# Kernel optimization log

Measured on AMD Instinct MI355X. Metric: run time of the kernel, lower is better.

## Reference

```python
import jax, jax.numpy as jnp
import numpy as np

N_NODES = 1024
N_FEAT = 12        # must equal LOOKBACK (U1 @ B @ U2.T constraint in original code)
LOOKBACK = 12
N_DATA = 8
KSIZE = 2
DILATIONS = [1, 3, 3, 3]
DELTA_MIN = 0.05
TIME_FEATS = 36    # 15 + 5 + 4 + 12


def setup_inputs() -> dict:
    key = jax.random.key(0)
    ks = jax.random.split(key, 21)
    f32 = jnp.float32

    def rn(k, shape, fan_in):
        return jax.random.normal(k, shape, dtype=f32) / np.sqrt(fan_in)

    return {
        'observation': jax.random.normal(ks[0], (N_NODES, N_DATA, LOOKBACK), dtype=f32),
        'time_features': jax.random.normal(ks[1], (TIME_FEATS,), dtype=f32),
        # main FC stack: (n_nodes*n_data) -> fc1 -> fc2 -> n_nodes*n_feat
        'fc_w1': rn(ks[2], (N_NODES * N_DATA, 2048), N_NODES * N_DATA),
        'fc_b1': jnp.zeros((2048,), f32),
        'fc_w2': rn(ks[3], (2048, 2048), 2048),
        'fc_b2': jnp.zeros((2048,), f32),
        'fc_w3': rn(ks[4], (2048, N_NODES * N_FEAT), 2048),
        'fc_b3': jnp.zeros((N_NODES * N_FEAT,), f32),
        # graph conv weights
        'W_forward': rn(ks[5], (KSIZE, N_FEAT, N_FEAT), N_FEAT),
        'W_backward': rn(ks[6], (KSIZE, N_FEAT, N_FEAT), N_FEAT),
        'b': jnp.zeros((N_FEAT,), f32),
        # GraphConstructor params (one fixed set, reused for every adjacency)
        'layer_initial': rn(ks[7], (LOOKBACK, N_NODES), N_NODES),
        'gs_w1': rn(ks[8], (N_NODES, 256), N_NODES),
        'gs_b1': jnp.zeros((256,), f32),
        'gs_w2': rn(ks[9], (256, N_NODES * N_FEAT), 256),
        'gs_b2': jnp.zeros((N_NODES * N_FEAT,), f32),
        'gt_w1': rn(ks[10], (TIME_FEATS, 256), TIME_FEATS),
        'gt_b1': jnp.zeros((256,), f32),
        'gt_w2': rn(ks[11], (256, N_NODES * N_FEAT), 256),
        'gt_b2': jnp.zeros((N_NODES * N_FEAT,), f32),
        'B': jax.random.normal(ks[12], (N_FEAT, N_FEAT), dtype=f32) / N_FEAT,
    }


def _forward(observation, time_features, fc_w1, fc_b1, fc_w2, fc_b2, fc_w3, fc_b3,
             W_forward, W_backward, b, layer_initial,
             gs_w1, gs_b1, gs_w2, gs_b2, gt_w1, gt_b1, gt_w2, gt_b2, B):
    relu = jax.nn.relu

    # fully_connected: observation (N, D, L) -> X (N, F, L)
    obs = jnp.transpose(observation, (2, 0, 1)).reshape(LOOKBACK, -1)  # (L, N*D)
    h = relu(obs @ fc_w1 + fc_b1)
    h = relu(h @ fc_w2 + fc_b2)
    h = relu(h @ fc_w3 + fc_b3)                                        # (L, N*F)
    X0 = jnp.transpose(h.reshape(LOOKBACK, N_NODES, N_FEAT), (1, 2, 0))  # (N, F, L)

    # node embedding U (N, L, F), computed once (graph params fixed)
    sp = relu(relu(layer_initial @ gs_w1 + gs_b1) @ gs_w2 + gs_b2)     # (L, N*F)
    tp = relu(relu(time_features @ gt_w1 + gt_b1) @ gt_w2 + gt_b2)     # (N*F,)
    U = jnp.transpose((sp + tp).reshape(LOOKBACK, N_NODES, N_FEAT), (1, 0, 2))

    adj_cache = {}

    def norm_adj(a, c):
        # normalized adjacency between feature-slices a and c (static ints)
        if (a, c) in adj_cache:
            return adj_cache[(a, c)]
        U1 = U[:, :, a]                      # (N, L)
        U2 = U[:, :, c]                      # (N, L)
        x = U1 @ B @ U2.T                    # (N, N); valid since L == F
        x = jnp.where(x >= DELTA_MIN, x, 0.0)
        A = jax.nn.softmax(x, axis=1)        # torch F.softmax default dim=1 for 2D
        # degree = diag(rowsum); inv(sqrtm(diag)) = diag(1/sqrt(rowsum))
        d = 1.0 / jnp.sqrt(A.sum(-1))
        out = A * d[:, None] * d[None, :]
        adj_cache[(a, c)] = out
        return out

    def conv(X, t):
        Z = jnp.zeros((N_NODES, N_FEAT), jnp.float32)
        for k in range(KSIZE):
            X_t = X[:, :, t - k]             # (N, F)
            L1 = norm_adj(t - k, t)
            L2 = norm_adj(t + k, t)
            x = L1 @ X_t @ W_forward[k] + L2 @ X_t @ W_backward[k] + b
            Z = Z + jax.nn.relu(x)
        return Z

    def conv_layer(X, d):
        cols = []
        for t in range(1, LOOKBACK - 1):
            if t % d == 0:
                cols.append(conv(X, t))
            else:
                cols.append(jnp.zeros((N_NODES, N_FEAT), jnp.float32))
        return jnp.stack(cols, axis=-1)      # (N, F, L-2)

    Z0 = conv_layer(X0, DILATIONS[0])
    Z1 = conv_layer(Z0, DILATIONS[1])
    Z2 = conv_layer(Z1, DILATIONS[2])
    Z3 = conv_layer(Z2, DILATIONS[3])
    return (Z0[:, :, -1], Z1[:, :, -1], Z2[:, :, -1], Z3[:, :, -1])


def reference(observation, time_features, fc_w1, fc_b1, fc_w2, fc_b2, fc_w3, fc_b3,
              W_forward, W_backward, b, layer_initial,
              gs_w1, gs_b1, gs_w2, gs_b2, gt_w1, gt_b1, gt_w2, gt_b2, B):
    return _forward(observation, time_features, fc_w1, fc_b1, fc_w2, fc_b2, fc_w3, fc_b3,
                    W_forward, W_backward, b, layer_initial,
                    gs_w1, gs_b1, gs_w2, gs_b2, gt_w1, gt_b1, gt_w2, gt_b2, B)
```

## Files before the change

kernel.cpp:

```cpp
#include <hip/hip_runtime.h>


#define OFF_SPP   0
#define OFF_TPH   49152
#define OFF_P1    65536
#define OFF_P2    196608
#define OFF_P3    262144
#define OFF_UP    393216
#define OFF_TPP   1572864
#define OFF_U     1703936
#define OFF_Y     1740800

template<int KS, int PIN, int P, int GATHER>
__device__ __forceinline__ void gemm_body(
    const float* __restrict__ xin, const float* __restrict__ bias_in,
    const float* __restrict__ W, float* __restrict__ part,
    int N, int K, int bx, int by, float* lx, float* red)
{
  int tid = threadIdx.x;
  int k0 = by * KS;
  for (int i = tid; i < 2*KS; i += 256) {
    int t = i / KS, kk = i - t*KS;
    float v;
    if (GATHER) {
      int k = k0 + kk;
      v = xin[(k >> 3)*96 + (k & 7)*12 + 9 + t];
    } else if (PIN == 0) {
      v = xin[t*K + k0 + kk];
    } else {
      v = 0.f;
      const float* p0 = xin + (size_t)(t*K + k0 + kk)*PIN;
      #pragma unroll
      for (int p = 0; p < PIN; ++p) v += p0[p];
    }
    if (bias_in) { v += bias_in[k0 + kk]; v = v > 0.f ? v : 0.f; }
    lx[i] = v;
  }
  __syncthreads();
  int kg = tid >> 5, cg = tid & 31;
  int colbase = bx*128 + cg*4;
  float a0=0,a1=0,a2=0,a3=0,c0=0,c1=0,c2=0,c3=0;
  const int ksub = KS/8;
  for (int kk = kg*ksub; kk < kg*ksub + ksub; ++kk) {
    float4 w = *(const float4*)(W + (size_t)(k0+kk)*N + colbase);
    float x0 = lx[kk], x1 = lx[KS + kk];
    a0=fmaf(x0,w.x,a0); a1=fmaf(x0,w.y,a1); a2=fmaf(x0,w.z,a2); a3=fmaf(x0,w.w,a3);
    c0=fmaf(x1,w.x,c0); c1=fmaf(x1,w.y,c1); c2=fmaf(x1,w.z,c2); c3=fmaf(x1,w.w,c3);
  }
  float* rp = red + (kg*32 + cg)*8;
  rp[0]=a0; rp[1]=a1; rp[2]=a2; rp[3]=a3; rp[4]=c0; rp[5]=c1; rp[6]=c2; rp[7]=c3;
  __syncthreads();
  int cg2 = tid & 31, q = tid >> 5;
  float s = 0.f;
  #pragma unroll
  for (int g = 0; g < 8; ++g) s += red[(g*32 + cg2)*8 + q];
  int t = q >> 2, c = q & 3;
  part[(size_t)(t*N + bx*128 + cg2*4 + c)*P + by] = s;
}

template<int KS, int PIN, int P>
__global__ void __launch_bounds__(256) k_gemm(
    const float* __restrict__ xin, const float* __restrict__ bias_in,
    const float* __restrict__ W, float* __restrict__ part, int N, int K)
{
  __shared__ float lx[2*KS];
  __shared__ float red[2048];
  gemm_body<KS, PIN, P, 0>(xin, bias_in, W, part, N, K,
                           blockIdx.x, blockIdx.y, lx, red);
}

__global__ void __launch_bounds__(256) k_front(
    const float* __restrict__ obs, const float* __restrict__ fc_w1,
    float* __restrict__ part1,
    const float* __restrict__ li, const float* __restrict__ gs_w1,
    const float* __restrict__ tf, const float* __restrict__ gt_w1,
    const float* __restrict__ gt_b1,
    float* __restrict__ sp_part, float* __restrict__ tp_h)
{
  __shared__ float smem[2560];
  int b = blockIdx.x, tid = threadIdx.x;
  if (b < 512) {
    gemm_body<256, 0, 32, 1>(obs, (const float*)nullptr, fc_w1, part1,
                             2048, 8192, b & 15, b >> 4, smem, smem + 512);
  } else if (b < 528) {
    float (*lil)[128] = (float(*)[128])smem;
    int sb = b - 512;
    int cb = sb & 1, kc = sb >> 1;
    for (int i = tid; i < 1536; i += 256) {
      int bb = i >> 7, kk = i & 127;
      lil[bb][kk] = li[bb*1024 + kc*128 + kk];
    }
    __syncthreads();
    int col = cb*128 + (tid & 127);
    int kh = tid >> 7;
    float acc[12];
    #pragma unroll
    for (int t=0;t<12;++t) acc[t]=0.f;
    for (int kk = kh*64; kk < kh*64 + 64; ++kk) {
      float w = gs_w1[(size_t)(kc*128 + kk)*256 + col];
      #pragma unroll
      for (int t=0;t<12;++t) acc[t] = fmaf(lil[t][kk], w, acc[t]);
    }
    int c = kc*2 + kh;
    #pragma unroll
    for (int t=0;t<12;++t) sp_part[(c*12 + t)*256 + col] = acc[t];
  } else {
    float acc = 0.f;
    for (int k = 0; k < 36; ++k)
      acc = fmaf(tf[k], gt_w1[k*256 + tid], acc);
    float v = acc + gt_b1[tid];
    tp_h[tid] = v > 0.f ? v : 0.f;
  }
}

__global__ void __launch_bounds__(256) k_big(
    const float* __restrict__ part2, const float* __restrict__ fc_b2,
    const float* __restrict__ fc_w3, float* __restrict__ part3,
    const float* __restrict__ sp_part, const float* __restrict__ gs_b1,
    const float* __restrict__ tp_h,
    const float* __restrict__ gs_w2, const float* __restrict__ gt_w2,
    float* __restrict__ U_part, float* __restrict__ tp_part)
{
  __shared__ float smem[3072];
  int g = blockIdx.x, tid = threadIdx.x;
  if (g < 384) {
    gemm_body<512, 16, 4, 0>(part2, fc_b2, fc_w3, part3, 12288, 2048,
                             g >> 2, g & 3, smem, smem + 1024);
  } else {
    float* spl = smem;
    float* tpl = smem + 96;
    int ug = g - 384;
    int n  = (ug & 3)*256 + tid;
    int uy = ug >> 2;
    int k0 = uy*8;
    if (tid < 96) {
      int kk = tid / 12, t = tid % 12;
      float v = gs_b1[k0 + kk];
      #pragma unroll
      for (int c = 0; c < 16; ++c) v += sp_part[(c*12 + t)*256 + k0 + kk];
      spl[kk*12 + t] = v > 0.f ? v : 0.f;
    }
    if (tid < 8) tpl[tid] = tp_h[k0 + tid];
    __syncthreads();
    float sA[3][12];
    float tA[3] = {0.f, 0.f, 0.f};
    #pragma unroll
    for (int ap=0;ap<3;++ap)
      #pragma unroll
      for (int t=0;t<12;++t) sA[ap][t]=0.f;
    #pragma unroll
    for (int kk = 0; kk < 8; ++kk) {
      float4 ws4 = *(const float4*)(gs_w2 + (size_t)(k0+kk)*12288 + 12*n + 8);
      float4 wt4 = *(const float4*)(gt_w2 + (size_t)(k0+kk)*12288 + 12*n + 8);
      float w0 = ws4.y, w1 = ws4.z, w2 = ws4.w;
      #pragma unroll
      for (int t=0;t<12;++t) {
        float s = spl[kk*12 + t];
        sA[0][t] = fmaf(s, w0, sA[0][t]);
        sA[1][t] = fmaf(s, w1, sA[1][t]);
        sA[2][t] = fmaf(s, w2, sA[2][t]);
      }
      float tv = tpl[kk];
      tA[0] = fmaf(tv, wt4.y, tA[0]);
      tA[1] = fmaf(tv, wt4.z, tA[1]);
      tA[2] = fmaf(tv, wt4.w, tA[2]);
    }
    #pragma unroll
    for (int ap=0;ap<3;++ap) {
      #pragma unroll
      for (int t=0;t<12;++t)
        U_part[(size_t)uy*36864 + ap*12288 + n*12 + t] = sA[ap][t];
      tp_part[uy*3072 + n*3 + ap] = tA[ap];
    }
  }
}

__global__ void __launch_bounds__(256) k_mid(
    const float* __restrict__ U_part, const float* __restrict__ tp_part,
    const float* __restrict__ gs_b2, const float* __restrict__ gt_b2,
    float* __restrict__ U,
    const float* __restrict__ part3, const float* __restrict__ fc_b3,
    const float* __restrict__ Wf, const float* __restrict__ Wb,
    float* __restrict__ Y, float* __restrict__ out_tail)
{
  int b = blockIdx.x, tid = threadIdx.x;
  if (b < 144) {
    int i = b*256 + tid;
    float us = 0.f;
    for (int y = 0; y < 32; ++y) us += U_part[(size_t)y*36864 + i];
    int ap = i / 12288, rem = i - ap*12288, n = rem / 12;
    float ts = 0.f;
    for (int y = 0; y < 32; ++y) ts += tp_part[y*3072 + n*3 + ap];
    int c = n*12 + 9 + ap;
    float sv = us + gs_b2[c]; sv = sv > 0.f ? sv : 0.f;
    float tv = ts + gt_b2[c]; tv = tv > 0.f ? tv : 0.f;
    U[i] = sv + tv;
  } else if (b < 148) {
    __shared__ float Ws0[144], Ws1[144], Ws2[144];
    if (tid < 144) {
      Ws0[tid] = Wf[144 + tid];
      Ws1[tid] = Wf[tid] + Wb[tid];
      Ws2[tid] = Wb[144 + tid];
    }
    __syncthreads();
    int n = (b - 144)*256 + tid;
    float X9[12], X10[12];
    #pragma unroll
    for (int f=0; f<12; ++f) {
      float bb = fc_b3[n*12 + f];
      const float* p9  = part3 + (size_t)(n*12 + f)*4;
      const float* p10 = part3 + (size_t)(12288 + n*12 + f)*4;
      float v9 = bb, v10 = bb;
      #pragma unroll
      for (int p = 0; p < 4; ++p) { v9 += p9[p]; v10 += p10[p]; }
      X9[f]  = v9  > 0.f ? v9  : 0.f;
      X10[f] = v10 > 0.f ? v10 : 0.f;
    }
    #pragma unroll
    for (int g2=0; g2<12; ++g2) {
      float y0=0.f, y1=0.f, y2=0.f;
      #pragma unroll
      for (int f=0; f<12; ++f) {
        y0 = fmaf(X9[f],  Ws0[f*12+g2], y0);
        y1 = fmaf(X10[f], Ws1[f*12+g2], y1);
        y2 = fmaf(X9[f],  Ws2[f*12+g2], y2);
      }
      Y[n*12 + g2]         = y0;
      Y[12288 + n*12 + g2] = y1;
      Y[24576 + n*12 + g2] = y2;
    }
  } else {
    int i = (b - 148)*256 + tid;
    out_tail[i] = 0.f;
  }
}

#define SS 1032
__global__ void __launch_bounds__(256) k_final(
    const float* __restrict__ U, const float* __restrict__ Y,
    const float* __restrict__ Bm, const float* __restrict__ bvec,
    float* __restrict__ out)
{
  __shared__ float sc[6*SS];
  __shared__ float P[2][3][12];
  __shared__ float invS[6];
  __shared__ float Bl[144];
  __shared__ float bl[12];
  int tid = threadIdx.x;
  int i0 = blockIdx.x*2;
  if (tid < 144) Bl[tid] = Bm[tid];
  if (tid < 12)  bl[tid] = bvec[tid];
  __syncthreads();
  if (tid < 72) {
    int r = tid / 36, ap = (tid / 12) % 3, j = tid % 12;
    float s = 0.f;
    #pragma unroll
    for (int t=0;t<12;++t)
      s = fmaf(U[ap*12288 + (i0+r)*12 + t], Bl[t*12 + j], s);
    P[r][ap][j] = s;
  }
  __syncthreads();
  const float* U10 = U + 12288;
  for (int jj = 0; jj < 4; ++jj) {
    int j = tid + jj*256;
    const float4* ur = (const float4*)(U10 + j*12);
    float4 u0 = ur[0], u1 = ur[1], u2 = ur[2];
    float u[12] = {u0.x,u0.y,u0.z,u0.w,u1.x,u1.y,u1.z,u1.w,u2.x,u2.y,u2.z,u2.w};
    #pragma unroll
    for (int r=0;r<2;++r)
      #pragma unroll
      for (int ap=0;ap<3;++ap) {
        float s = 0.f;
        #pragma unroll
        for (int t=0;t<12;++t) s = fmaf(P[r][ap][t], u[t], s);
        sc[(r*3+ap)*SS + j] = (s >= 0.05f) ? s : 0.f;
      }
  }
  __syncthreads();
  int wv = tid >> 6, ln = tid & 63;
  for (int p = wv; p < 6; p += 4) {
    float m = -1e30f;
    for (int q = 0; q < 16; ++q) m = fmaxf(m, sc[p*SS + ln + q*64]);
    #pragma unroll
    for (int o = 32; o > 0; o >>= 1) m = fmaxf(m, __shfl_xor(m, o));
    float sum = 0.f;
    for (int q = 0; q < 16; ++q) {
      int j = ln + q*64;
      float e = __expf(sc[p*SS + j] - m);
      sc[p*SS + j] = e;
      sum += e;
    }
    #pragma unroll
    for (int o = 32; o > 0; o >>= 1) sum += __shfl_xor(sum, o);
    if (ln == 0) invS[p] = 1.f / sum;
  }
  __syncthreads();
  float acc[2][12];
  for (int r = 0; r < 2; ++r)
    for (int f = 0; f < 12; ++f)
      acc[r][f] = 0.f;
  int q3 = tid >> 6, jg = tid & 63;
  if (tid < 192) {
    for (int q = 0; q < 16; ++q) {
      int j = jg + q*64;
      const float4* yr = (const float4*)(Y + q3*12288 + j*12);
      float4 y0 = yr[0], y1 = yr[1], y2 = yr[2];
      float yv[12] = {y0.x,y0.y,y0.z,y0.w,y1.x,y1.y,y1.z,y1.w,y2.x,y2.y,y2.z,y2.w};
      float e0 = sc[(0*3+q3)*SS + j];
      float e1 = sc[(1*3+q3)*SS + j];
      #pragma unroll
      for (int f=0;f<12;++f) {
        acc[0][f] = fmaf(e0, yv[f], acc[0][f]);
        acc[1][f] = fmaf(e1, yv[f], acc[1][f]);
      }
    }
  }
  __syncthreads();
  float* red = sc;
  if (tid < 192) {
    #pragma unroll
    for (int r=0;r<2;++r)
      #pragma unroll
      for (int f=0;f<12;++f)
        red[((q3*2 + r)*12 + f)*64 + jg] = acc[r][f];
  }
  __syncthreads();
  if (tid < 24) {
    int r = tid / 12, f = tid % 12;
    float s0=0.f, s1=0.f, s2=0.f;
    for (int g = 0; g < 64; ++g) {
      s0 += red[((0*2+r)*12+f)*64 + g];
      s1 += red[((1*2+r)*12+f)*64 + g];
      s2 += red[((2*2+r)*12+f)*64 + g];
    }
    float a1v = invS[r*3+1]*s1;
    float a2v = invS[r*3+0]*s0 + invS[r*3+2]*s2;
    float v1 = a1v + bl[f]; v1 = v1>0.f ? v1 : 0.f;
    float v2 = a2v + bl[f]; v2 = v2>0.f ? v2 : 0.f;
    out[(i0+r)*12 + f] = v1 + v2;
  }
}

extern "C" void kernel_launch(void* const* d_in, const int* in_sizes, int n_in,
                              void* d_out, int out_size, void* d_ws, size_t ws_size,
                              hipStream_t stream)
{
  const float* obs   = (const float*)d_in[0];
  const float* tf    = (const float*)d_in[1];
  const float* fc_w1 = (const float*)d_in[2];
  const float* fc_b1 = (const float*)d_in[3];
  const float* fc_w2 = (const float*)d_in[4];
  const float* fc_b2 = (const float*)d_in[5];
  const float* fc_w3 = (const float*)d_in[6];
  const float* fc_b3 = (const float*)d_in[7];
  const float* Wf    = (const float*)d_in[8];
  const float* Wb    = (const float*)d_in[9];
  const float* bvec  = (const float*)d_in[10];
  const float* li    = (const float*)d_in[11];
  const float* gs_w1 = (const float*)d_in[12];
  const float* gs_b1 = (const float*)d_in[13];
  const float* gs_w2 = (const float*)d_in[14];
  const float* gs_b2 = (const float*)d_in[15];
  const float* gt_w1 = (const float*)d_in[16];
  const float* gt_b1 = (const float*)d_in[17];
  const float* gt_w2 = (const float*)d_in[18];
  const float* gt_b2 = (const float*)d_in[19];
  const float* Bm    = (const float*)d_in[20];
  float* out = (float*)d_out;
  float* ws  = (float*)d_ws;

  float* sp_part = ws + OFF_SPP;
  float* tp_h    = ws + OFF_TPH;
  float* part1   = ws + OFF_P1;
  float* part2   = ws + OFF_P2;
  float* part3   = ws + OFF_P3;
  float* U_part  = ws + OFF_UP;
  float* tp_part = ws + OFF_TPP;
  float* U       = ws + OFF_U;
  float* Y       = ws + OFF_Y;

  k_front<<<dim3(529), dim3(256), 0, stream>>>(obs, fc_w1, part1,
                                               li, gs_w1, tf, gt_w1, gt_b1,
                                               sp_part, tp_h);
  k_gemm<128, 32, 16><<<dim3(16,16), dim3(256), 0, stream>>>(
      part1, fc_b1, fc_w2, part2, 2048, 2048);
  k_big<<<dim3(512), dim3(256), 0, stream>>>(part2, fc_b2, fc_w3, part3,
                                             sp_part, gs_b1, tp_h,
                                             gs_w2, gt_w2, U_part, tp_part);
  k_mid<<<dim3(292), dim3(256), 0, stream>>>(U_part, tp_part, gs_b2, gt_b2, U,
                                             part3, fc_b3, Wf, Wb, Y,
                                             out + 12288);
  k_final<<<dim3(512), dim3(256), 0, stream>>>(U, Y, Bm, bvec, out);
}
```

Measured before the change: 294.7 us.

## Restructure pipeline into four kernels, fusing U computation and softmax with GEMMs

```diff
diff --git a/kernel.cpp b/kernel.cpp
--- a/kernel.cpp
+++ b/kernel.cpp
@@ -1,15 +1,13 @@
 #include <hip/hip_runtime.h>
-
 
 #define OFF_SPP   0
 #define OFF_TPH   49152
 #define OFF_P1    65536
 #define OFF_P2    196608
 #define OFF_P3    262144
-#define OFF_UP    393216
-#define OFF_TPP   1572864
 #define OFF_U     1703936
-#define OFF_Y     1740800
+#define OFF_E     1777664
+#define OFF_IS    4923392
 
 template<int KS, int PIN, int P, int GATHER>
 __device__ __forceinline__ void gemm_body(
@@ -31,14 +29,14 @@
       v = 0.f;
       const float* p0 = xin + (size_t)(t*K + k0 + kk)*PIN;
       #pragma unroll
-      for (int p = 0; p < PIN; ++p) v += p0[p];
+      for (int pp = 0; pp < PIN; ++pp) v += p0[pp];
     }
     if (bias_in) { v += bias_in[k0 + kk]; v = v > 0.f ? v : 0.f; }
     lx[i] = v;
   }
   __syncthreads();
-  int kg = tid >> 5, cg = tid & 31;
-  int colbase = bx*128 + cg*4;
+  int kg = tid >> 5, cg2 = tid & 31;
+  int colbase = bx*128 + cg2*4;
   float a0=0,a1=0,a2=0,a3=0,c0=0,c1=0,c2=0,c3=0;
   const int ksub = KS/8;
   for (int kk = kg*ksub; kk < kg*ksub + ksub; ++kk) {
@@ -47,26 +45,15 @@
     a0=fmaf(x0,w.x,a0); a1=fmaf(x0,w.y,a1); a2=fmaf(x0,w.z,a2); a3=fmaf(x0,w.w,a3);
     c0=fmaf(x1,w.x,c0); c1=fmaf(x1,w.y,c1); c2=fmaf(x1,w.z,c2); c3=fmaf(x1,w.w,c3);
   }
-  float* rp = red + (kg*32 + cg)*8;
+  float* rp = red + (kg*32 + cg2)*8;
   rp[0]=a0; rp[1]=a1; rp[2]=a2; rp[3]=a3; rp[4]=c0; rp[5]=c1; rp[6]=c2; rp[7]=c3;
   __syncthreads();
-  int cg2 = tid & 31, q = tid >> 5;
+  int cg3 = tid & 31, q = tid >> 5;
   float s = 0.f;
   #pragma unroll
-  for (int g = 0; g < 8; ++g) s += red[(g*32 + cg2)*8 + q];
+  for (int g = 0; g < 8; ++g) s += red[(g*32 + cg3)*8 + q];
   int t = q >> 2, c = q & 3;
-  part[(size_t)(t*N + bx*128 + cg2*4 + c)*P + by] = s;
-}
-
-template<int KS, int PIN, int P>
-__global__ void __launch_bounds__(256) k_gemm(
-    const float* __restrict__ xin, const float* __restrict__ bias_in,
-    const float* __restrict__ W, float* __restrict__ part, int N, int K)
-{
-  __shared__ float lx[2*KS];
-  __shared__ float red[2048];
-  gemm_body<KS, PIN, P, 0>(xin, bias_in, W, part, N, K,
-                           blockIdx.x, blockIdx.y, lx, red);
+  part[(size_t)(t*N + bx*128 + cg3*4 + c)*P + by] = s;
 }
 
 __global__ void __launch_bounds__(256) k_front(
@@ -75,7 +62,8 @@
     const float* __restrict__ li, const float* __restrict__ gs_w1,
     const float* __restrict__ tf, const float* __restrict__ gt_w1,
     const float* __restrict__ gt_b1,
-    float* __restrict__ sp_part, float* __restrict__ tp_h)
+    float* __restrict__ sp_part, float* __restrict__ tp_h,
+    float* __restrict__ out_tail)
 {
   __shared__ float smem[2560];
   int b = blockIdx.x, tid = threadIdx.x;
@@ -87,8 +75,8 @@
     int sb = b - 512;
     int cb = sb & 1, kc = sb >> 1;
     for (int i = tid; i < 1536; i += 256) {
-      int bb = i >> 7, kk = i & 127;
-      lil[bb][kk] = li[bb*1024 + kc*128 + kk];
+      int r = i >> 7, kk = i & 127;
+      lil[r][kk] = li[r*1024 + kc*128 + kk];
     }
     __syncthreads();
     int col = cb*128 + (tid & 127);
@@ -104,6 +92,7 @@
     int c = kc*2 + kh;
     #pragma unroll
     for (int t=0;t<12;++t) sp_part[(c*12 + t)*256 + col] = acc[t];
+    for (int i = tid; i < 2304; i += 256) out_tail[sb*2304 + i] = 0.f;
   } else {
     float acc = 0.f;
     for (int k = 0; k < 36; ++k)
@@ -113,210 +102,182 @@
   }
 }
 
-__global__ void __launch_bounds__(256) k_big(
-    const float* __restrict__ part2, const float* __restrict__ fc_b2,
-    const float* __restrict__ fc_w3, float* __restrict__ part3,
+__global__ void __launch_bounds__(256) k_umid(
+    const float* __restrict__ part1, const float* __restrict__ fc_b1,
+    const float* __restrict__ fc_w2, float* __restrict__ part2,
     const float* __restrict__ sp_part, const float* __restrict__ gs_b1,
     const float* __restrict__ tp_h,
     const float* __restrict__ gs_w2, const float* __restrict__ gt_w2,
-    float* __restrict__ U_part, float* __restrict__ tp_part)
-{
-  __shared__ float smem[3072];
-  int g = blockIdx.x, tid = threadIdx.x;
-  if (g < 384) {
+    const float* __restrict__ gs_b2, const float* __restrict__ gt_b2,
+    float* __restrict__ U)
+{
+  __shared__ float smem[3328];
+  int b = blockIdx.x, tid = threadIdx.x;
+  if (b < 256) {
+    gemm_body<128, 32, 16, 0>(part1, fc_b1, fc_w2, part2, 2048, 2048,
+                              b & 15, b >> 4, smem, smem + 256);
+    return;
+  }
+  float* spl = smem;
+  float* tpl = smem + 3072;
+  for (int i = tid; i < 3072; i += 256) {
+    int k = i / 12, t = i - k*12;
+    float v = gs_b1[k];
+    #pragma unroll
+    for (int c = 0; c < 16; ++c) v += sp_part[(c*12 + t)*256 + k];
+    spl[i] = v > 0.f ? v : 0.f;
+  }
+  tpl[tid] = tp_h[tid];
+  __syncthreads();
+  int grp = tid >> 5, l = tid & 31;
+  int n = (b - 256)*8 + grp;
+  int ap1 = l / 12, t1 = l - ap1*12;
+  bool has2 = (l < 7), sp2 = (l < 4);
+  int t2 = 8 + l;
+  const float* g1 = gs_w2 + 12*n + 9 + ap1;
+  const float* g2 = sp2 ? (gs_w2 + 12*n + 11)
+                        : (has2 ? (gt_w2 + 12*n + 9 + (l - 4)) : gs_w2);
+  float a1 = 0.f, a2 = 0.f;
+  #pragma unroll 8
+  for (int k = 0; k < 256; ++k) {
+    float w1 = g1[(size_t)k*12288];
+    a1 = fmaf(spl[k*12 + t1], w1, a1);
+    if (has2) {
+      float w2 = g2[(size_t)k*12288];
+      float x2 = sp2 ? spl[k*12 + t2] : tpl[k];
+      a2 = fmaf(x2, w2, a2);
+    }
+  }
+  float tp0 = __shfl(a2, 4, 32);
+  float tp1 = __shfl(a2, 5, 32);
+  float tp2 = __shfl(a2, 6, 32);
+  float tpv = (ap1 == 0) ? tp0 : ((ap1 == 1) ? tp1 : tp2);
+  int c1 = n*12 + 9 + ap1;
+  float sv = a1 + gs_b2[c1]; sv = sv > 0.f ? sv : 0.f;
+  float tv = tpv + gt_b2[c1]; tv = tv > 0.f ? tv : 0.f;
+  U[ap1*12288 + n*12 + t1] = sv + tv;
+  if (sp2) {
+    int c2 = n*12 + 11;
+    float sv2 = a2 + gs_b2[c2]; sv2 = sv2 > 0.f ? sv2 : 0.f;
+    float tv2 = tp2 + gt_b2[c2]; tv2 = tv2 > 0.f ? tv2 : 0.f;
+    U[2*12288 + n*12 + t2] = sv2 + tv2;
+  }
+}
+
+#define SS 1032
+__global__ void __launch_bounds__(256) k_sfc3(
+    const float* __restrict__ part2, const float* __restrict__ fc_b2,
+    const float* __restrict__ fc_w3, float* __restrict__ part3,
+    const float* __restrict__ U, const float* __restrict__ Bm,
+    float* __restrict__ E, float* __restrict__ invSg)
+{
+  __shared__ float smem[6448];
+  int b = blockIdx.x, tid = threadIdx.x;
+  if (b < 384) {
     gemm_body<512, 16, 4, 0>(part2, fc_b2, fc_w3, part3, 12288, 2048,
-                             g >> 2, g & 3, smem, smem + 1024);
-  } else {
-    float* spl = smem;
-    float* tpl = smem + 96;
-    int ug = g - 384;
-    int n  = (ug & 3)*256 + tid;
-    int uy = ug >> 2;
-    int k0 = uy*8;
-    if (tid < 96) {
-      int kk = tid / 12, t = tid % 12;
-      float v = gs_b1[k0 + kk];
-      #pragma unroll
-      for (int c = 0; c < 16; ++c) v += sp_part[(c*12 + t)*256 + k0 + kk];
-      spl[kk*12 + t] = v > 0.f ? v : 0.f;
-    }
-    if (tid < 8) tpl[tid] = tp_h[k0 + tid];
+                             b >> 2, b & 3, smem, smem + 1024);
+    return;
+  }
+  float* sc = smem;
+  float* Pm = smem + 6192;
+  float* Bl = smem + 6264;
+  int sb = b - 384;
+  if (tid < 144) Bl[tid] = Bm[tid];
+  __syncthreads();
+  const float* U10 = U + 12288;
+  for (int pp = 0; pp < 4; ++pp) {
+    int pair = sb*4 + pp;
+    int i0 = pair*2;
+    if (tid < 72) {
+      int r = tid / 36, ap = (tid / 12) % 3, j = tid % 12;
+      float s = 0.f;
+      #pragma unroll
+      for (int t=0;t<12;++t)
+        s = fmaf(U[ap*12288 + (i0+r)*12 + t], Bl[t*12 + j], s);
+      Pm[(r*3+ap)*12 + j] = s;
+    }
     __syncthreads();
-    float sA[3][12];
-    float tA[3] = {0.f, 0.f, 0.f};
-    #pragma unroll
-    for (int ap=0;ap<3;++ap)
-      #pragma unroll
-      for (int t=0;t<12;++t) sA[ap][t]=0.f;
-    #pragma unroll
-    for (int kk = 0; kk < 8; ++kk) {
-      float4 ws4 = *(const float4*)(gs_w2 + (size_t)(k0+kk)*12288 + 12*n + 8);
-      float4 wt4 = *(const float4*)(gt_w2 + (size_t)(k0+kk)*12288 + 12*n + 8);
-      float w0 = ws4.y, w1 = ws4.z, w2 = ws4.w;
-      #pragma unroll
-      for (int t=0;t<12;++t) {
-        float s = spl[kk*12 + t];
-        sA[0][t] = fmaf(s, w0, sA[0][t]);
-        sA[1][t] = fmaf(s, w1, sA[1][t]);
-        sA[2][t] = fmaf(s, w2, sA[2][t]);
+    for (int jj = 0; jj < 4; ++jj) {
+      int j = tid + jj*256;
+      const float4* ur = (const float4*)(U10 + j*12);
+      float4 u0 = ur[0], u1 = ur[1], u2 = ur[2];
+      float u[12] = {u0.x,u0.y,u0.z,u0.w,u1.x,u1.y,u1.z,u1.w,u2.x,u2.y,u2.z,u2.w};
+      #pragma unroll
+      for (int r=0;r<2;++r)
+        #pragma unroll
+        for (int ap=0;ap<3;++ap) {
+          float s = 0.f;
+          #pragma unroll
+          for (int t=0;t<12;++t) s = fmaf(Pm[(r*3+ap)*12 + t], u[t], s);
+          sc[(r*3+ap)*SS + j] = (s >= 0.05f) ? s : 0.f;
+        }
+    }
+    __syncthreads();
+    int wv = tid >> 6, ln = tid & 63;
+    for (int pr = wv; pr < 6; pr += 4) {
+      float m = -1e30f;
+      for (int q = 0; q < 16; ++q) m = fmaxf(m, sc[pr*SS + ln + q*64]);
+      #pragma unroll
+      for (int o = 32; o > 0; o >>= 1) m = fmaxf(m, __shfl_xor(m, o));
+      float sum = 0.f;
+      for (int q = 0; q < 16; ++q) {
+        int j = ln + q*64;
+        float e = __expf(sc[pr*SS + j] - m);
+        E[(size_t)pair*6144 + pr*1024 + j] = e;
+        sum += e;
       }
-      float tv = tpl[kk];
-      tA[0] = fmaf(tv, wt4.y, tA[0]);
-      tA[1] = fmaf(tv, wt4.z, tA[1]);
-      tA[2] = fmaf(tv, wt4.w, tA[2]);
-    }
-    #pragma unroll
-    for (int ap=0;ap<3;++ap) {
-      #pragma unroll
-      for (int t=0;t<12;++t)
-        U_part[(size_t)uy*36864 + ap*12288 + n*12 + t] = sA[ap][t];
-      tp_part[uy*3072 + n*3 + ap] = tA[ap];
-    }
-  }
-}
-
-__global__ void __launch_bounds__(256) k_mid(
-    const float* __restrict__ U_part, const float* __restrict__ tp_part,
-    const float* __restrict__ gs_b2, const float* __restrict__ gt_b2,
-    float* __restrict__ U,
+      #pragma unroll
+      for (int o = 32; o > 0; o >>= 1) sum += __shfl_xor(sum, o);
+      if (ln == 0) invSg[pair*6 + pr] = 1.f / sum;
+    }
+    __syncthreads();
+  }
+}
+
+__global__ void __launch_bounds__(256) k_out(
+    const float* __restrict__ E, const float* __restrict__ invSg,
     const float* __restrict__ part3, const float* __restrict__ fc_b3,
     const float* __restrict__ Wf, const float* __restrict__ Wb,
-    float* __restrict__ Y, float* __restrict__ out_tail)
-{
+    const float* __restrict__ bvec, float* __restrict__ out)
+{
+  __shared__ float red[4608];
+  __shared__ float Ws0[144], Ws1[144], Ws2[144];
+  __shared__ float wbuf[72];
+  __shared__ float invS[6], bl[12];
   int b = blockIdx.x, tid = threadIdx.x;
-  if (b < 144) {
-    int i = b*256 + tid;
-    float us = 0.f;
-    for (int y = 0; y < 32; ++y) us += U_part[(size_t)y*36864 + i];
-    int ap = i / 12288, rem = i - ap*12288, n = rem / 12;
-    float ts = 0.f;
-    for (int y = 0; y < 32; ++y) ts += tp_part[y*3072 + n*3 + ap];
-    int c = n*12 + 9 + ap;
-    float sv = us + gs_b2[c]; sv = sv > 0.f ? sv : 0.f;
-    float tv = ts + gt_b2[c]; tv = tv > 0.f ? tv : 0.f;
-    U[i] = sv + tv;
-  } else if (b < 148) {
-    __shared__ float Ws0[144], Ws1[144], Ws2[144];
-    if (tid < 144) {
-      Ws0[tid] = Wf[144 + tid];
-      Ws1[tid] = Wf[tid] + Wb[tid];
-      Ws2[tid] = Wb[144 + tid];
-    }
-    __syncthreads();
-    int n = (b - 144)*256 + tid;
-    float X9[12], X10[12];
-    #pragma unroll
-    for (int f=0; f<12; ++f) {
-      float bb = fc_b3[n*12 + f];
-      const float* p9  = part3 + (size_t)(n*12 + f)*4;
-      const float* p10 = part3 + (size_t)(12288 + n*12 + f)*4;
-      float v9 = bb, v10 = bb;
-      #pragma unroll
-      for (int p = 0; p < 4; ++p) { v9 += p9[p]; v10 += p10[p]; }
-      X9[f]  = v9  > 0.f ? v9  : 0.f;
-      X10[f] = v10 > 0.f ? v10 : 0.f;
-    }
-    #pragma unroll
-    for (int g2=0; g2<12; ++g2) {
-      float y0=0.f, y1=0.f, y2=0.f;
-      #pragma unroll
-      for (int f=0; f<12; ++f) {
-        y0 = fmaf(X9[f],  Ws0[f*12+g2], y0);
-        y1 = fmaf(X10[f], Ws1[f*12+g2], y1);
-        y2 = fmaf(X9[f],  Ws2[f*12+g2], y2);
-      }
-      Y[n*12 + g2]         = y0;
-      Y[12288 + n*12 + g2] = y1;
-      Y[24576 + n*12 + g2] = y2;
-    }
-  } else {
-    int i = (b - 148)*256 + tid;
-    out_tail[i] = 0.f;
-  }
-}
-
-#define SS 1032
-__global__ void __launch_bounds__(256) k_final(
-    const float* __restrict__ U, const float* __restrict__ Y,
-    const float* __restrict__ Bm, const float* __restrict__ bvec,
-    float* __restrict__ out)
-{
-  __shared__ float sc[6*SS];
-  __shared__ float P[2][3][12];
-  __shared__ float invS[6];
-  __shared__ float Bl[144];
-  __shared__ float bl[12];
-  int tid = threadIdx.x;
-  int i0 = blockIdx.x*2;
-  if (tid < 144) Bl[tid] = Bm[tid];
-  if (tid < 12)  bl[tid] = bvec[tid];
-  __syncthreads();
-  if (tid < 72) {
-    int r = tid / 36, ap = (tid / 12) % 3, j = tid % 12;
-    float s = 0.f;
-    #pragma unroll
-    for (int t=0;t<12;++t)
-      s = fmaf(U[ap*12288 + (i0+r)*12 + t], Bl[t*12 + j], s);
-    P[r][ap][j] = s;
-  }
-  __syncthreads();
-  const float* U10 = U + 12288;
-  for (int jj = 0; jj < 4; ++jj) {
-    int j = tid + jj*256;
-    const float4* ur = (const float4*)(U10 + j*12);
-    float4 u0 = ur[0], u1 = ur[1], u2 = ur[2];
-    float u[12] = {u0.x,u0.y,u0.z,u0.w,u1.x,u1.y,u1.z,u1.w,u2.x,u2.y,u2.z,u2.w};
-    #pragma unroll
-    for (int r=0;r<2;++r)
-      #pragma unroll
-      for (int ap=0;ap<3;++ap) {
-        float s = 0.f;
-        #pragma unroll
-        for (int t=0;t<12;++t) s = fmaf(P[r][ap][t], u[t], s);
-        sc[(r*3+ap)*SS + j] = (s >= 0.05f) ? s : 0.f;
-      }
-  }
-  __syncthreads();
-  int wv = tid >> 6, ln = tid & 63;
-  for (int p = wv; p < 6; p += 4) {
-    float m = -1e30f;
-    for (int q = 0; q < 16; ++q) m = fmaxf(m, sc[p*SS + ln + q*64]);
-    #pragma unroll
-    for (int o = 32; o > 0; o >>= 1) m = fmaxf(m, __shfl_xor(m, o));
-    float sum = 0.f;
-    for (int q = 0; q < 16; ++q) {
-      int j = ln + q*64;
-      float e = __expf(sc[p*SS + j] - m);
-      sc[p*SS + j] = e;
-      sum += e;
-    }
-    #pragma unroll
-    for (int o = 32; o > 0; o >>= 1) sum += __shfl_xor(sum, o);
-    if (ln == 0) invS[p] = 1.f / sum;
-  }
-  __syncthreads();
+  if (tid < 144) {
+    Ws0[tid] = Wf[144 + tid];
+    Ws1[tid] = Wf[tid] + Wb[tid];
+    Ws2[tid] = Wb[144 + tid];
+  }
+  if (tid < 6)  invS[tid] = invSg[b*6 + tid];
+  if (tid < 12) bl[tid]   = bvec[tid];
   float acc[2][12];
-  for (int r = 0; r < 2; ++r)
-    for (int f = 0; f < 12; ++f)
-      acc[r][f] = 0.f;
+  #pragma unroll
+  for (int r=0;r<2;++r)
+    #pragma unroll
+    for (int f=0;f<12;++f) acc[r][f] = 0.f;
   int q3 = tid >> 6, jg = tid & 63;
   if (tid < 192) {
+    const float* Eb = E + (size_t)b*6144;
+    int row = (q3 == 1) ? 1 : 0;
+    const float* p3r = part3 + (size_t)row*49152;
     for (int q = 0; q < 16; ++q) {
       int j = jg + q*64;
-      const float4* yr = (const float4*)(Y + q3*12288 + j*12);
-      float4 y0 = yr[0], y1 = yr[1], y2 = yr[2];
-      float yv[12] = {y0.x,y0.y,y0.z,y0.w,y1.x,y1.y,y1.z,y1.w,y2.x,y2.y,y2.z,y2.w};
-      float e0 = sc[(0*3+q3)*SS + j];
-      float e1 = sc[(1*3+q3)*SS + j];
-      #pragma unroll
-      for (int f=0;f<12;++f) {
-        acc[0][f] = fmaf(e0, yv[f], acc[0][f]);
-        acc[1][f] = fmaf(e1, yv[f], acc[1][f]);
+      float e0 = Eb[q3*1024 + j];
+      float e1 = Eb[(3 + q3)*1024 + j];
+      const float4* px = (const float4*)(p3r + (size_t)j*48);
+      const float* bb = fc_b3 + j*12;
+      #pragma unroll
+      for (int f = 0; f < 12; ++f) {
+        float4 v4 = px[f];
+        float x = v4.x + v4.y + v4.z + v4.w + bb[f];
+        x = x > 0.f ? x : 0.f;
+        acc[0][f] = fmaf(e0, x, acc[0][f]);
+        acc[1][f] = fmaf(e1, x, acc[1][f]);
       }
     }
   }
-  __syncthreads();
-  float* red = sc;
   if (tid < 192) {
     #pragma unroll
     for (int r=0;r<2;++r)
@@ -325,19 +286,27 @@
         red[((q3*2 + r)*12 + f)*64 + jg] = acc[r][f];
   }
   __syncthreads();
+  if (tid < 72) {
+    int q3b = tid / 24, rr = (tid / 12) % 2, f = tid % 12;
+    float s = 0.f;
+    for (int g = 0; g < 64; ++g) s += red[((q3b*2 + rr)*12 + f)*64 + g];
+    wbuf[(q3b*2 + rr)*12 + f] = s;
+  }
+  __syncthreads();
   if (tid < 24) {
-    int r = tid / 12, f = tid % 12;
-    float s0=0.f, s1=0.f, s2=0.f;
-    for (int g = 0; g < 64; ++g) {
-      s0 += red[((0*2+r)*12+f)*64 + g];
-      s1 += red[((1*2+r)*12+f)*64 + g];
-      s2 += red[((2*2+r)*12+f)*64 + g];
-    }
-    float a1v = invS[r*3+1]*s1;
-    float a2v = invS[r*3+0]*s0 + invS[r*3+2]*s2;
-    float v1 = a1v + bl[f]; v1 = v1>0.f ? v1 : 0.f;
-    float v2 = a2v + bl[f]; v2 = v2>0.f ? v2 : 0.f;
-    out[(i0+r)*12 + f] = v1 + v2;
+    int r = tid / 12, g = tid % 12;
+    float y0=0.f, y1=0.f, y2=0.f;
+    #pragma unroll
+    for (int f=0; f<12; ++f) {
+      y0 = fmaf(wbuf[(0*2+r)*12+f], Ws0[f*12+g], y0);
+      y1 = fmaf(wbuf[(1*2+r)*12+f], Ws1[f*12+g], y1);
+      y2 = fmaf(wbuf[(2*2+r)*12+f], Ws2[f*12+g], y2);
+    }
+    float a1v = invS[r*3+1]*y1;
+    float a2v = invS[r*3+0]*y0 + invS[r*3+2]*y2;
+    float v1 = a1v + bl[g]; v1 = v1>0.f ? v1 : 0.f;
+    float v2 = a2v + bl[g]; v2 = v2>0.f ? v2 : 0.f;
+    out[(b*2+r)*12 + g] = v1 + v2;
   }
 }
 
@@ -374,21 +343,18 @@
   float* part1   = ws + OFF_P1;
   float* part2   = ws + OFF_P2;
   float* part3   = ws + OFF_P3;
-  float* U_part  = ws + OFF_UP;
-  float* tp_part = ws + OFF_TPP;
   float* U       = ws + OFF_U;
-  float* Y       = ws + OFF_Y;
+  float* E       = ws + OFF_E;
+  float* invSg   = ws + OFF_IS;
 
   k_front<<<dim3(529), dim3(256), 0, stream>>>(obs, fc_w1, part1,
                                                li, gs_w1, tf, gt_w1, gt_b1,
-                                               sp_part, tp_h);
-  k_gemm<128, 32, 16><<<dim3(16,16), dim3(256), 0, stream>>>(
-      part1, fc_b1, fc_w2, part2, 2048, 2048);
-  k_big<<<dim3(512), dim3(256), 0, stream>>>(part2, fc_b2, fc_w3, part3,
-                                             sp_part, gs_b1, tp_h,
-                                             gs_w2, gt_w2, U_part, tp_part);
-  k_mid<<<dim3(292), dim3(256), 0, stream>>>(U_part, tp_part, gs_b2, gt_b2, U,
-                                             part3, fc_b3, Wf, Wb, Y,
-                                             out + 12288);
-  k_final<<<dim3(512), dim3(256), 0, stream>>>(U, Y, Bm, bvec, out);
-}
+                                               sp_part, tp_h, out + 12288);
+  k_umid<<<dim3(384), dim3(256), 0, stream>>>(part1, fc_b1, fc_w2, part2,
+                                              sp_part, gs_b1, tp_h,
+                                              gs_w2, gt_w2, gs_b2, gt_b2, U);
+  k_sfc3<<<dim3(512), dim3(256), 0, stream>>>(part2, fc_b2, fc_w3, part3,
+                                              U, Bm, E, invSg);
+  k_out<<<dim3(512), dim3(256), 0, stream>>>(E, invSg, part3, fc_b3,
+                                             Wf, Wb, bvec, out);
+}
```

Measured after the change: 424.1 us. +43.9%, slower.
